# Kernel tuning notes

Hardware: AMD Instinct MI355X
Metric: run time of the kernel (lower is better)

Reference implementation:

```python
import jax, jax.numpy as jnp
import numpy as np

BATCH = 512
IN_FLAT = 1024
NEURONS = 4096
FOCUS = 64


def setup_inputs() -> dict:
    key = jax.random.key(0)
    k1, k2, k3, k4 = jax.random.split(key, 4)
    x = jax.random.normal(k1, (BATCH, IN_FLAT), dtype=jnp.float32)
    connections_index = jax.random.randint(k2, (NEURONS, FOCUS), 0, IN_FLAT, dtype=jnp.int64)
    weights = jax.random.normal(k3, (NEURONS, FOCUS), dtype=jnp.float32)
    bias = jax.random.normal(k4, (NEURONS,), dtype=jnp.float32)
    return {"x": x, "connections_index": connections_index, "weights": weights, "bias": bias}


def reference(x, connections_index, weights, bias):
    # x: [B, IN_FLAT]; gather fixed sparse indices per output neuron
    # x_sel: [B, NEURONS, FOCUS]
    x_sel = jnp.take(x, connections_index, axis=1)
    # elementwise multiply by learned weights and reduce over focus dim
    y = jnp.sum(x_sel * weights, axis=-1) + bias  # [B, NEURONS]
    return y.reshape(x.shape[0], NEURONS)
```

## Files before the change

kernel.cpp:

```cpp
#include <hip/hip_runtime.h>

#define IN_FLAT 1024
#define BATCH   512
#define NEURONS 4096
#define FOCUS   64
#define BT      8

__device__ __forceinline__ unsigned short f32_to_bf16(float f) {
    unsigned int u = __float_as_uint(f);
    unsigned int r = (u + 0x7fffu + ((u >> 16) & 1u)) >> 16;
    return (unsigned short)r;
}

__global__ __launch_bounds__(256) void transpose_bf16_kernel(
        const float* __restrict__ x, unsigned short* __restrict__ xt2) {
    __shared__ float tile[32][33];
    const int i0 = blockIdx.x * 32;
    const int b0 = blockIdx.y * 32;
    const int t  = threadIdx.x;

    {
        const int r  = t >> 3;
        const int c4 = t & 7;
        float4 v = *reinterpret_cast<const float4*>(
            x + (size_t)(b0 + r) * IN_FLAT + i0 + c4 * 4);
        tile[r][c4 * 4 + 0] = v.x;
        tile[r][c4 * 4 + 1] = v.y;
        tile[r][c4 * 4 + 2] = v.z;
        tile[r][c4 * 4 + 3] = v.w;
    }
    __syncthreads();

    {
        const int il = t >> 3;
        const int q  = t & 7;
        ushort4 o;
        o.x = f32_to_bf16(tile[q * 4 + 0][il]);
        o.y = f32_to_bf16(tile[q * 4 + 1][il]);
        o.z = f32_to_bf16(tile[q * 4 + 2][il]);
        o.w = f32_to_bf16(tile[q * 4 + 3][il]);
        const int chunk  = (b0 >> 3) + (q >> 1);
        const int within = (q & 1) * 4;
        size_t off = (size_t)chunk * IN_FLAT * BT + (size_t)(i0 + il) * BT + within;
        *reinterpret_cast<ushort4*>(xt2 + off) = o;
    }
}

__global__ __launch_bounds__(256) void gather_dot_kernel(
        const unsigned short* __restrict__ xt2,
        const int*   __restrict__ idx,
        const float* __restrict__ w,
        const float* __restrict__ bias,
        float*       __restrict__ y) {
    __shared__ unsigned short lxt[IN_FLAT * BT];

    const int nb = blockIdx.x;
    const int bb = blockIdx.y;
    const int t  = threadIdx.x;

    {
        const uint4* src = reinterpret_cast<const uint4*>(
            xt2 + (size_t)bb * IN_FLAT * BT);
        uint4* dst = reinterpret_cast<uint4*>(lxt);
        #pragma unroll
        for (int u = 0; u < 4; ++u)
            dst[u * 256 + t] = src[u * 256 + t];
    }
    __syncthreads();

    const int n = nb * 256 + t;
    float acc[BT];
    #pragma unroll
    for (int k = 0; k < BT; ++k) acc[k] = 0.f;

    const int*   ip = idx + (size_t)n * FOCUS;
    const float* wp = w   + (size_t)n * FOCUS;

    #pragma unroll 4
    for (int f4 = 0; f4 < FOCUS / 4; ++f4) {
        const int4   i4 = *reinterpret_cast<const int4*>(ip + f4 * 4);
        const float4 w4 = *reinterpret_cast<const float4*>(wp + f4 * 4);
        const int   iv[4] = {i4.x, i4.y, i4.z, i4.w};
        const float wv[4] = {w4.x, w4.y, w4.z, w4.w};
        #pragma unroll
        for (int j = 0; j < 4; ++j) {
            const int i = iv[j] & (IN_FLAT - 1);
            const float ww = wv[j];
            const uint4 r = *reinterpret_cast<const uint4*>(lxt + i * BT);
            acc[0] += ww * __uint_as_float(r.x << 16);
            acc[1] += ww * __uint_as_float(r.x & 0xffff0000u);
            acc[2] += ww * __uint_as_float(r.y << 16);
            acc[3] += ww * __uint_as_float(r.y & 0xffff0000u);
            acc[4] += ww * __uint_as_float(r.z << 16);
            acc[5] += ww * __uint_as_float(r.z & 0xffff0000u);
            acc[6] += ww * __uint_as_float(r.w << 16);
            acc[7] += ww * __uint_as_float(r.w & 0xffff0000u);
        }
    }

    const float bv = bias[n];
    const int b0 = bb * BT;
    #pragma unroll
    for (int k = 0; k < BT; ++k) {
        y[(size_t)(b0 + k) * NEURONS + n] = acc[k] + bv;
    }
}

extern "C" void kernel_launch(void* const* d_in, const int* in_sizes, int n_in,
                              void* d_out, int out_size, void* d_ws, size_t ws_size,
                              hipStream_t stream) {
    const float* x    = (const float*)d_in[0];
    const int*   idx  = (const int*)  d_in[1];
    const float* w    = (const float*)d_in[2];
    const float* bias = (const float*)d_in[3];
    float*       y    = (float*)d_out;

    unsigned short* xt2 = (unsigned short*)d_ws;

    transpose_bf16_kernel<<<dim3(IN_FLAT / 32, BATCH / 32), 256, 0, stream>>>(x, xt2);
    gather_dot_kernel<<<dim3(NEURONS / 256, BATCH / BT), 256, 0, stream>>>(
        xt2, idx, w, bias, y);
}
```

Measured before the change: 82.45 us.

## Use fp32 planar x layout and pre-packed coalesced index/weight pairs

Drops the bf16 conversion and keeps x transposed in fp32, split into two 4-float planes per batch chunk so each gather is two float4 LDS reads. A new pre-pass kernel packs index (as a byte offset) and weight into interleaved pairs laid out so a thread reads two focus elements per coalesced uint4 load, instead of each thread striding through its own row of idx and w. This removes the per-element bf16 unpacking and the uncoalesced per-thread reads, but doubles the LDS tile to 32KB (which can lower occupancy), doubles the transposed-x traffic, and adds a third kernel launch.

```diff
diff --git a/kernel.cpp b/kernel.cpp
--- a/kernel.cpp
+++ b/kernel.cpp
@@ -5,15 +5,12 @@
 #define NEURONS 4096
 #define FOCUS   64
 #define BT      8
+#define CHUNK_FLOATS (IN_FLAT * BT)
+#define PLANE_FLOATS (IN_FLAT * 4)
+#define PLANE_BYTES  (PLANE_FLOATS * 4)
 
-__device__ __forceinline__ unsigned short f32_to_bf16(float f) {
-    unsigned int u = __float_as_uint(f);
-    unsigned int r = (u + 0x7fffu + ((u >> 16) & 1u)) >> 16;
-    return (unsigned short)r;
-}
-
-__global__ __launch_bounds__(256) void transpose_bf16_kernel(
-        const float* __restrict__ x, unsigned short* __restrict__ xt2) {
+__global__ __launch_bounds__(256) void transpose_f32_kernel(
+        const float* __restrict__ x, float* __restrict__ xt) {
     __shared__ float tile[32][33];
     const int i0 = blockIdx.x * 32;
     const int b0 = blockIdx.y * 32;
@@ -34,25 +31,39 @@
     {
         const int il = t >> 3;
         const int q  = t & 7;
-        ushort4 o;
-        o.x = f32_to_bf16(tile[q * 4 + 0][il]);
-        o.y = f32_to_bf16(tile[q * 4 + 1][il]);
-        o.z = f32_to_bf16(tile[q * 4 + 2][il]);
-        o.w = f32_to_bf16(tile[q * 4 + 3][il]);
-        const int chunk  = (b0 >> 3) + (q >> 1);
-        const int within = (q & 1) * 4;
-        size_t off = (size_t)chunk * IN_FLAT * BT + (size_t)(i0 + il) * BT + within;
-        *reinterpret_cast<ushort4*>(xt2 + off) = o;
+        float4 o;
+        o.x = tile[q * 4 + 0][il];
+        o.y = tile[q * 4 + 1][il];
+        o.z = tile[q * 4 + 2][il];
+        o.w = tile[q * 4 + 3][il];
+        const int chunk = (b0 >> 3) + (q >> 1);
+        const int plane = q & 1;
+        float* dst = xt + (size_t)chunk * CHUNK_FLOATS + plane * PLANE_FLOATS
+                        + (size_t)(i0 + il) * 4;
+        *reinterpret_cast<float4*>(dst) = o;
     }
 }
 
+__global__ __launch_bounds__(256) void pack_pw_kernel(
+        const int* __restrict__ idx, const float* __restrict__ w,
+        uint2* __restrict__ pw) {
+    const int tid = blockIdx.x * 256 + threadIdx.x;
+    const int n = tid >> 6;
+    const int f = tid & 63;
+    const int i = idx[tid] & (IN_FLAT - 1);
+    uint2 e;
+    e.x = (unsigned)(i * 16);
+    e.y = __float_as_uint(w[tid]);
+    const int dst = ((n >> 8) * 32 + (f >> 1)) * 512 + (n & 255) * 2 + (f & 1);
+    pw[dst] = e;
+}
+
 __global__ __launch_bounds__(256) void gather_dot_kernel(
-        const unsigned short* __restrict__ xt2,
-        const int*   __restrict__ idx,
-        const float* __restrict__ w,
+        const float* __restrict__ xt,
+        const uint4* __restrict__ pw4,
         const float* __restrict__ bias,
         float*       __restrict__ y) {
-    __shared__ unsigned short lxt[IN_FLAT * BT];
+    __shared__ float lx[CHUNK_FLOATS];
 
     const int nb = blockIdx.x;
     const int bb = blockIdx.y;
@@ -60,44 +71,41 @@
 
     {
         const uint4* src = reinterpret_cast<const uint4*>(
-            xt2 + (size_t)bb * IN_FLAT * BT);
-        uint4* dst = reinterpret_cast<uint4*>(lxt);
+            xt + (size_t)bb * CHUNK_FLOATS);
+        uint4* dst = reinterpret_cast<uint4*>(lx);
         #pragma unroll
-        for (int u = 0; u < 4; ++u)
+        for (int u = 0; u < 8; ++u)
             dst[u * 256 + t] = src[u * 256 + t];
     }
     __syncthreads();
 
-    const int n = nb * 256 + t;
     float acc[BT];
     #pragma unroll
     for (int k = 0; k < BT; ++k) acc[k] = 0.f;
 
-    const int*   ip = idx + (size_t)n * FOCUS;
-    const float* wp = w   + (size_t)n * FOCUS;
+    const uint4* pt = pw4 + (size_t)nb * 8192;
+    const char*  lxb = reinterpret_cast<const char*>(lx);
 
     #pragma unroll 4
-    for (int f4 = 0; f4 < FOCUS / 4; ++f4) {
-        const int4   i4 = *reinterpret_cast<const int4*>(ip + f4 * 4);
-        const float4 w4 = *reinterpret_cast<const float4*>(wp + f4 * 4);
-        const int   iv[4] = {i4.x, i4.y, i4.z, i4.w};
-        const float wv[4] = {w4.x, w4.y, w4.z, w4.w};
-        #pragma unroll
-        for (int j = 0; j < 4; ++j) {
-            const int i = iv[j] & (IN_FLAT - 1);
-            const float ww = wv[j];
-            const uint4 r = *reinterpret_cast<const uint4*>(lxt + i * BT);
-            acc[0] += ww * __uint_as_float(r.x << 16);
-            acc[1] += ww * __uint_as_float(r.x & 0xffff0000u);
-            acc[2] += ww * __uint_as_float(r.y << 16);
-            acc[3] += ww * __uint_as_float(r.y & 0xffff0000u);
-            acc[4] += ww * __uint_as_float(r.z << 16);
-            acc[5] += ww * __uint_as_float(r.z & 0xffff0000u);
-            acc[6] += ww * __uint_as_float(r.w << 16);
-            acc[7] += ww * __uint_as_float(r.w & 0xffff0000u);
-        }
+    for (int f2 = 0; f2 < 32; ++f2) {
+        const uint4 p = pt[f2 * 256 + t];
+        const float4 a0 = *reinterpret_cast<const float4*>(lxb + p.x);
+        const float4 b0 = *reinterpret_cast<const float4*>(lxb + p.x + PLANE_BYTES);
+        const float4 a1 = *reinterpret_cast<const float4*>(lxb + p.z);
+        const float4 b1 = *reinterpret_cast<const float4*>(lxb + p.z + PLANE_BYTES);
+        const float w0 = __uint_as_float(p.y);
+        const float w1 = __uint_as_float(p.w);
+        acc[0] += w0 * a0.x;  acc[1] += w0 * a0.y;
+        acc[2] += w0 * a0.z;  acc[3] += w0 * a0.w;
+        acc[4] += w0 * b0.x;  acc[5] += w0 * b0.y;
+        acc[6] += w0 * b0.z;  acc[7] += w0 * b0.w;
+        acc[0] += w1 * a1.x;  acc[1] += w1 * a1.y;
+        acc[2] += w1 * a1.z;  acc[3] += w1 * a1.w;
+        acc[4] += w1 * b1.x;  acc[5] += w1 * b1.y;
+        acc[6] += w1 * b1.z;  acc[7] += w1 * b1.w;
     }
 
+    const int n  = nb * 256 + t;
     const float bv = bias[n];
     const int b0 = bb * BT;
     #pragma unroll
@@ -115,9 +123,11 @@
     const float* bias = (const float*)d_in[3];
     float*       y    = (float*)d_out;
 
-    unsigned short* xt2 = (unsigned short*)d_ws;
+    float* xt = (float*)d_ws;
+    uint2* pw = (uint2*)((char*)d_ws + (size_t)BATCH * IN_FLAT * 4);
 
-    transpose_bf16_kernel<<<dim3(IN_FLAT / 32, BATCH / 32), 256, 0, stream>>>(x, xt2);
+    transpose_f32_kernel<<<dim3(IN_FLAT / 32, BATCH / 32), 256, 0, stream>>>(x, xt);
+    pack_pw_kernel<<<dim3(NEURONS * FOCUS / 256), 256, 0, stream>>>(idx, w, pw);
     gather_dot_kernel<<<dim3(NEURONS / 256, BATCH / BT), 256, 0, stream>>>(
-        xt2, idx, w, bias, y);
+        xt, (const uint4*)pw, bias, y);
 }
```

New measurement: 83.10 us. About the same (+0.8%).

## Recast sparse gather-dot as dense bf16 MFMA GEMM via scattered weight matrix

Applied to the files above, without the earlier changes.

Each call now scatters the sparse per-neuron weights into a dense bf16 matrix of shape [NEURONS, IN_FLAT], using shared-memory atomics to sum duplicate indices. It converts x to bf16 and runs a tiled MFMA GEMM with double-buffered, swizzled LDS tiles and an XCD-aware block mapping. This replaces the scalar LDS gather and FMA loop with matrix-core work, but performs 16x more arithmetic on mostly-zero weights. It also writes and reads an 8 MB dense weight matrix through HBM on every call.

```diff
diff --git a/kernel.cpp b/kernel.cpp
--- a/kernel.cpp
+++ b/kernel.cpp
@@ -4,105 +4,154 @@
 #define BATCH   512
 #define NEURONS 4096
 #define FOCUS   64
-#define BT      8
+
+typedef __bf16 bf16x8 __attribute__((ext_vector_type(8)));
+typedef float  f32x4  __attribute__((ext_vector_type(4)));
 
 __device__ __forceinline__ unsigned short f32_to_bf16(float f) {
     unsigned int u = __float_as_uint(f);
     unsigned int r = (u + 0x7fffu + ((u >> 16) & 1u)) >> 16;
     return (unsigned short)r;
 }
+__device__ __forceinline__ unsigned int pack2(float a, float b) {
+    return (unsigned int)f32_to_bf16(a) | ((unsigned int)f32_to_bf16(b) << 16);
+}
 
-__global__ __launch_bounds__(256) void transpose_bf16_kernel(
-        const float* __restrict__ x, unsigned short* __restrict__ xt2) {
-    __shared__ float tile[32][33];
-    const int i0 = blockIdx.x * 32;
-    const int b0 = blockIdx.y * 32;
+__global__ __launch_bounds__(256) void build_wt_kernel(
+        const int* __restrict__ idx, const float* __restrict__ w,
+        unsigned short* __restrict__ Wt) {
+    __shared__ float rb[8 * IN_FLAT];
     const int t  = threadIdx.x;
+    const int g0 = blockIdx.x * 8;
 
-    {
-        const int r  = t >> 3;
-        const int c4 = t & 7;
-        float4 v = *reinterpret_cast<const float4*>(
-            x + (size_t)(b0 + r) * IN_FLAT + i0 + c4 * 4);
-        tile[r][c4 * 4 + 0] = v.x;
-        tile[r][c4 * 4 + 1] = v.y;
-        tile[r][c4 * 4 + 2] = v.z;
-        tile[r][c4 * 4 + 3] = v.w;
+    float4* rb4 = reinterpret_cast<float4*>(rb);
+    #pragma unroll
+    for (int u = 0; u < 8; ++u)
+        rb4[u * 256 + t] = float4{0.f, 0.f, 0.f, 0.f};
+    __syncthreads();
+
+    const int base = g0 * FOCUS;
+    #pragma unroll
+    for (int p = t; p < 8 * FOCUS; p += 256) {
+        const int   i  = idx[base + p] & (IN_FLAT - 1);
+        const float ww = w[base + p];
+        atomicAdd(&rb[(p >> 6) * IN_FLAT + i], ww);
     }
     __syncthreads();
 
-    {
-        const int il = t >> 3;
-        const int q  = t & 7;
-        ushort4 o;
-        o.x = f32_to_bf16(tile[q * 4 + 0][il]);
-        o.y = f32_to_bf16(tile[q * 4 + 1][il]);
-        o.z = f32_to_bf16(tile[q * 4 + 2][il]);
-        o.w = f32_to_bf16(tile[q * 4 + 3][il]);
-        const int chunk  = (b0 >> 3) + (q >> 1);
-        const int within = (q & 1) * 4;
-        size_t off = (size_t)chunk * IN_FLAT * BT + (size_t)(i0 + il) * BT + within;
-        *reinterpret_cast<ushort4*>(xt2 + off) = o;
+    uint4* dst = reinterpret_cast<uint4*>(Wt + (size_t)g0 * IN_FLAT);
+    #pragma unroll
+    for (int c = 0; c < 4; ++c) {
+        const float4 lo = rb4[c * 512 + t * 2];
+        const float4 hi = rb4[c * 512 + t * 2 + 1];
+        dst[c * 256 + t] = uint4{pack2(lo.x, lo.y), pack2(lo.z, lo.w),
+                                 pack2(hi.x, hi.y), pack2(hi.z, hi.w)};
     }
 }
 
-__global__ __launch_bounds__(256) void gather_dot_kernel(
-        const unsigned short* __restrict__ xt2,
-        const int*   __restrict__ idx,
-        const float* __restrict__ w,
+__global__ __launch_bounds__(256) void convert_x_kernel(
+        const float* __restrict__ x, unsigned short* __restrict__ A) {
+    const int t = blockIdx.x * 256 + threadIdx.x;
+    const float4 lo = reinterpret_cast<const float4*>(x)[t * 2];
+    const float4 hi = reinterpret_cast<const float4*>(x)[t * 2 + 1];
+    reinterpret_cast<uint4*>(A)[t] = uint4{pack2(lo.x, lo.y), pack2(lo.z, lo.w),
+                                           pack2(hi.x, hi.y), pack2(hi.z, hi.w)};
+}
+
+__global__ __launch_bounds__(256) void gemm_kernel(
+        const unsigned short* __restrict__ A,
+        const unsigned short* __restrict__ W,
         const float* __restrict__ bias,
-        float*       __restrict__ y) {
-    __shared__ unsigned short lxt[IN_FLAT * BT];
+        float* __restrict__ y) {
+    __shared__ uint4 smem4[2048];
+    char* smem = reinterpret_cast<char*>(smem4);
 
-    const int nb = blockIdx.x;
-    const int bb = blockIdx.y;
-    const int t  = threadIdx.x;
+    const int b   = blockIdx.x;
+    const int xcd = b & 7, jj = b >> 3;
+    const int m0  = (jj & 7) * 64;
+    const int n0  = (xcd * 8 + (jj >> 3)) * 64;
 
-    {
-        const uint4* src = reinterpret_cast<const uint4*>(
-            xt2 + (size_t)bb * IN_FLAT * BT);
-        uint4* dst = reinterpret_cast<uint4*>(lxt);
+    const int tid  = threadIdx.x;
+    const int lane = tid & 63;
+    const int wv   = tid >> 6;
+    const int wr   = wv >> 1, wc = wv & 1;
+
+    const int s0 = tid * 16, s1 = s0 + 4096;
+    const int r0 = s0 >> 7,  r1 = s1 >> 7;
+    const int c0 = (s0 & 127) >> 1, c1 = (s1 & 127) >> 1;
+    const unsigned short* gA0 = A + (m0 + r0) * IN_FLAT + c0;
+    const unsigned short* gA1 = A + (m0 + r1) * IN_FLAT + c1;
+    const unsigned short* gB0 = W + (size_t)(n0 + r0) * IN_FLAT + c0;
+    const unsigned short* gB1 = W + (size_t)(n0 + r1) * IN_FLAT + c1;
+    const int dA0 = s0 ^ ((r0 & 7) << 4);
+    const int dA1 = s1 ^ ((r1 & 7) << 4);
+    const int dB0 = dA0 + 8192, dB1 = dA1 + 8192;
+
+    f32x4 acc[2][2] = {};
+    uint4 ra0, ra1, rb0, rb1;
+
+    ra0 = *reinterpret_cast<const uint4*>(gA0);
+    ra1 = *reinterpret_cast<const uint4*>(gA1);
+    rb0 = *reinterpret_cast<const uint4*>(gB0);
+    rb1 = *reinterpret_cast<const uint4*>(gB1);
+
+    for (int t = 0; t < IN_FLAT / 64; ++t) {
+        const int bb = (t & 1) << 14;
+        *reinterpret_cast<uint4*>(smem + bb + dA0) = ra0;
+        *reinterpret_cast<uint4*>(smem + bb + dA1) = ra1;
+        *reinterpret_cast<uint4*>(smem + bb + dB0) = rb0;
+        *reinterpret_cast<uint4*>(smem + bb + dB1) = rb1;
+        __syncthreads();
+
+        if (t < 15) {
+            const int k = (t + 1) * 64;
+            ra0 = *reinterpret_cast<const uint4*>(gA0 + k);
+            ra1 = *reinterpret_cast<const uint4*>(gA1 + k);
+            rb0 = *reinterpret_cast<const uint4*>(gB0 + k);
+            rb1 = *reinterpret_cast<const uint4*>(gB1 + k);
+        }
+
         #pragma unroll
-        for (int u = 0; u < 4; ++u)
-            dst[u * 256 + t] = src[u * 256 + t];
-    }
-    __syncthreads();
-
-    const int n = nb * 256 + t;
-    float acc[BT];
-    #pragma unroll
-    for (int k = 0; k < BT; ++k) acc[k] = 0.f;
-
-    const int*   ip = idx + (size_t)n * FOCUS;
-    const float* wp = w   + (size_t)n * FOCUS;
-
-    #pragma unroll 4
-    for (int f4 = 0; f4 < FOCUS / 4; ++f4) {
-        const int4   i4 = *reinterpret_cast<const int4*>(ip + f4 * 4);
-        const float4 w4 = *reinterpret_cast<const float4*>(wp + f4 * 4);
-        const int   iv[4] = {i4.x, i4.y, i4.z, i4.w};
-        const float wv[4] = {w4.x, w4.y, w4.z, w4.w};
-        #pragma unroll
-        for (int j = 0; j < 4; ++j) {
-            const int i = iv[j] & (IN_FLAT - 1);
-            const float ww = wv[j];
-            const uint4 r = *reinterpret_cast<const uint4*>(lxt + i * BT);
-            acc[0] += ww * __uint_as_float(r.x << 16);
-            acc[1] += ww * __uint_as_float(r.x & 0xffff0000u);
-            acc[2] += ww * __uint_as_float(r.y << 16);
-            acc[3] += ww * __uint_as_float(r.y & 0xffff0000u);
-            acc[4] += ww * __uint_as_float(r.z << 16);
-            acc[5] += ww * __uint_as_float(r.z & 0xffff0000u);
-            acc[6] += ww * __uint_as_float(r.w << 16);
-            acc[7] += ww * __uint_as_float(r.w & 0xffff0000u);
+        for (int ks = 0; ks < 2; ++ks) {
+            const int kb = ks * 64 + ((lane >> 4) << 4);
+            bf16x8 af[2], bfr[2];
+            #pragma unroll
+            for (int fm = 0; fm < 2; ++fm) {
+                const int row = wr * 32 + fm * 16 + (lane & 15);
+                const int L   = row * 128 + kb;
+                af[fm] = *reinterpret_cast<const bf16x8*>(
+                    smem + bb + (L ^ ((row & 7) << 4)));
+            }
+            #pragma unroll
+            for (int fn = 0; fn < 2; ++fn) {
+                const int row = wc * 32 + fn * 16 + (lane & 15);
+                const int L   = row * 128 + kb;
+                bfr[fn] = *reinterpret_cast<const bf16x8*>(
+                    smem + bb + 8192 + (L ^ ((row & 7) << 4)));
+            }
+            #pragma unroll
+            for (int fm = 0; fm < 2; ++fm)
+                #pragma unroll
+                for (int fn = 0; fn < 2; ++fn)
+                    acc[fm][fn] = __builtin_amdgcn_mfma_f32_16x16x32_bf16(
+                        af[fm], bfr[fn], acc[fm][fn], 0, 0, 0);
         }
+        __syncthreads();
     }
 
-    const float bv = bias[n];
-    const int b0 = bb * BT;
+    const int nbase = n0 + wc * 32 + (lane & 15);
+    const int mbase = m0 + wr * 32 + ((lane >> 4) << 2);
     #pragma unroll
-    for (int k = 0; k < BT; ++k) {
-        y[(size_t)(b0 + k) * NEURONS + n] = acc[k] + bv;
+    for (int fn = 0; fn < 2; ++fn) {
+        const float bv = bias[nbase + fn * 16];
+        #pragma unroll
+        for (int fm = 0; fm < 2; ++fm) {
+            #pragma unroll
+            for (int jr = 0; jr < 4; ++jr) {
+                y[(size_t)(mbase + fm * 16 + jr) * NEURONS + nbase + fn * 16] =
+                    acc[fm][fn][jr] + bv;
+            }
+        }
     }
 }
 
@@ -115,9 +164,10 @@
     const float* bias = (const float*)d_in[3];
     float*       y    = (float*)d_out;
 
-    unsigned short* xt2 = (unsigned short*)d_ws;
+    unsigned short* Wt = (unsigned short*)d_ws;
+    unsigned short* A  = (unsigned short*)((char*)d_ws + (size_t)NEURONS * IN_FLAT * 2);
 
-    transpose_bf16_kernel<<<dim3(IN_FLAT / 32, BATCH / 32), 256, 0, stream>>>(x, xt2);
-    gather_dot_kernel<<<dim3(NEURONS / 256, BATCH / BT), 256, 0, stream>>>(
-        xt2, idx, w, bias, y);
+    build_wt_kernel<<<NEURONS / 8, 256, 0, stream>>>(idx, w, Wt);
+    convert_x_kernel<<<BATCH * IN_FLAT / (256 * 8), 256, 0, stream>>>(x, A);
+    gemm_kernel<<<(BATCH / 64) * (NEURONS / 64), 256, 0, stream>>>(A, Wt, bias, y);
 }
```

After: 82.22 us. No clear change (-0.3%).
